# Kernel optimization log

Hardware: AMD Instinct MI355X
Metric: run time of the kernel (lower is better)

## Reference

```python
import jax, jax.numpy as jnp
import numpy as np

NUM_HEADS = 16
KEY_DIM = 64
EPS = 1e-6


def setup_inputs() -> dict:
    key = jax.random.key(0)
    k0, k1, k2, k3, k4 = jax.random.split(key, 5)
    B, S, E = 4, 4096, NUM_HEADS * KEY_DIM
    scale = 1.0 / np.sqrt(KEY_DIM)
    return {
        "query": jax.random.normal(k0, (B, S, E), dtype=jnp.float32),
        "Wq": jax.random.normal(k1, (NUM_HEADS, KEY_DIM, KEY_DIM), dtype=jnp.float32) * scale,
        "Wk": jax.random.normal(k2, (NUM_HEADS, KEY_DIM, KEY_DIM), dtype=jnp.float32) * scale,
        "Wv": jax.random.normal(k3, (NUM_HEADS, KEY_DIM, KEY_DIM), dtype=jnp.float32) * scale,
        "Wo": jax.random.normal(k4, (E, E), dtype=jnp.float32) * (1.0 / np.sqrt(E)),
    }


def reference(query, Wq, Wk, Wv, Wo):
    # Self-attention: key = value = query (per call() defaults).
    B, S, E = query.shape
    H, D = NUM_HEADS, KEY_DIM
    # split_heads: (B, S, E) -> (B, H, S, D)
    x = jnp.transpose(query.reshape(B, S, H, D), (0, 2, 1, 3))
    # Per-head linear projections (all heads batched in one einsum each).
    q = jnp.einsum("bhsd,hde->bhse", x, Wq)
    k = jnp.einsum("bhsd,hde->bhse", x, Wk)
    v = jnp.einsum("bhsd,hde->bhse", x, Wv)
    # Kernel feature map phi(x) = elu(x) + 1 (strictly positive).
    phi_q = jax.nn.elu(q) + 1.0
    phi_k = jax.nn.elu(k) + 1.0
    # Linear (non-causal) attention: O(S*D^2) instead of O(S^2*D).
    kv = jnp.einsum("bhsd,bhse->bhde", phi_k, v)        # (B,H,D,D)
    k_sum = jnp.sum(phi_k, axis=2)                       # (B,H,D)
    z = jnp.einsum("bhsd,bhd->bhs", phi_q, k_sum)        # (B,H,S)
    ctx = jnp.einsum("bhsd,bhde->bhse", phi_q, kv) / (z[..., None] + EPS)
    # combine_heads: (B,H,S,D) -> (B,S,E), then output projection (no bias).
    combined = jnp.transpose(ctx, (0, 2, 1, 3)).reshape(B, S, H * D)
    return combined @ Wo
```

## Files before the change

kernel.cpp:

```cpp
#include <hip/hip_runtime.h>
#include <stdint.h>

#define S_LEN 4096
#define NHEADS 16
#define DHEAD 64
#define EMB 1024
#define NBATCH 4
#define NBH (NBATCH * NHEADS)

typedef unsigned short u16t;
typedef __attribute__((ext_vector_type(8))) short short8;
typedef __attribute__((ext_vector_type(4))) float f32x4;

__device__ __forceinline__ u16t f2bf(float f) {
  unsigned int x = __float_as_uint(f);
  x += 0x7fffu + ((x >> 16) & 1u);
  return (u16t)(x >> 16);
}
__device__ __forceinline__ unsigned int pack2(float a, float b) {
  return (unsigned int)f2bf(a) | ((unsigned int)f2bf(b) << 16);
}
__device__ __forceinline__ float bf2f(u16t u) { return __uint_as_float(((unsigned int)u) << 16); }
__device__ __forceinline__ float phifn(float v) { return v > 0.f ? v + 1.f : __expf(v); }

__device__ __forceinline__ void stage_w8k(const u16t* __restrict__ wg,
                                          u16t* __restrict__ lds, int t) {
#pragma unroll
  for (int c = 0; c < 2; ++c) {
    const u16t* src = wg + (size_t)(c * 256 + t) * 8;
    char* dst = (char*)lds + c * 4096 + ((t >> 6) << 10);
    __builtin_amdgcn_global_load_lds((const __attribute__((address_space(1))) unsigned int*)src,
                                     (__attribute__((address_space(3))) unsigned int*)dst,
                                     16, 0, 0);
  }
}

__global__ __launch_bounds__(256) void la_prep(const float* __restrict__ Wq,
                                               const float* __restrict__ Wk,
                                               const float* __restrict__ Wv,
                                               u16t* __restrict__ WqT,
                                               u16t* __restrict__ WkT,
                                               u16t* __restrict__ WvT) {
  __shared__ float tmp[64][65];
  int blk = blockIdx.x;
  int mat = blk >> 4, h = blk & 15;
  const float* src = (mat == 0 ? Wq : (mat == 1 ? Wk : Wv)) + (size_t)h * 4096;
  u16t* dst = (mat == 0 ? WqT : (mat == 1 ? WkT : WvT)) + (size_t)h * 4096;
  int t = threadIdx.x;
#pragma unroll
  for (int p = 0; p < 16; ++p) {
    int i = p * 256 + t;
    tmp[i >> 6][i & 63] = src[i];
  }
  __syncthreads();
#pragma unroll
  for (int p = 0; p < 16; ++p) {
    int i = p * 256 + t;
    int e = i >> 6, r = i & 63, o = r >> 3, j = r & 7;
    dst[i] = f2bf(tmp[((o ^ (e & 7)) << 3) + j][e]);
  }
}

__global__ __launch_bounds__(256) void la_wot(const float* __restrict__ Wo,
                                              u16t* __restrict__ WoT) {
  __shared__ float t[64][65];
  int n0 = blockIdx.x * 64, k0 = blockIdx.y * 64;
  int tx = threadIdx.x, ty = threadIdx.y;
  for (int r = ty; r < 64; r += 4) t[r][tx] = Wo[(size_t)(k0 + r) * EMB + n0 + tx];
  __syncthreads();
  for (int r = ty; r < 64; r += 4)
    WoT[(size_t)(n0 + r) * EMB + k0 + tx] = f2bf(t[tx][r]);
}

__global__ __launch_bounds__(256) void la_kvq4(const float* __restrict__ q,
                                               const u16t* __restrict__ WqT,
                                               const u16t* __restrict__ WkT,
                                               const u16t* __restrict__ WvT,
                                               u16t* __restrict__ phiq,
                                               float* __restrict__ kvpart,
                                               float* __restrict__ kspart) {
  __shared__ u16t xs[128 * 72];
  __shared__ u16t wq[4096];
  __shared__ u16t wk[4096];
  __shared__ u16t wv[4096];
  __shared__ u16t pkT[64 * 136];
  __shared__ u16t vT[64 * 136];
  __shared__ float ksp4[4][64];
  int blk = blockIdx.x;
  int bh = blk >> 3, tile = blk & 7;
  int b = bh >> 4, h = bh & 15;
  int s0 = tile << 9;
  int t = threadIdx.x;
  int wave = t >> 6, lane = t & 63, l16 = lane & 15, g = lane >> 4;

  stage_w8k(WqT + (size_t)h * 4096, wq, t);
  stage_w8k(WkT + (size_t)h * 4096, wk, t);
  stage_w8k(WvT + (size_t)h * 4096, wv, t);

  const float* xg = q + ((size_t)b * S_LEN + s0) * EMB + h * 64;
  int pr_r = t >> 4, pr_c4 = (t & 15) * 4;

  float4 pre[8];
#pragma unroll
  for (int i = 0; i < 8; ++i)
    pre[i] = *(const float4*)(xg + (size_t)(i * 16 + pr_r) * EMB + pr_c4);

  f32x4 kacc[4];
#pragma unroll
  for (int n = 0; n < 4; ++n) kacc[n] = 0.f;
  float ks_acc = 0.f;
  int ks_e = t & 63, ks_q = t >> 6;

  for (int c = 0; c < 4; ++c) {
    if (c) __syncthreads();
#pragma unroll
    for (int i = 0; i < 8; ++i) {
      uint2 p;
      p.x = pack2(pre[i].x, pre[i].y);
      p.y = pack2(pre[i].z, pre[i].w);
      *(uint2*)(&xs[(i * 16 + pr_r) * 72 + pr_c4]) = p;
    }
    if (c < 3) {
#pragma unroll
      for (int i = 0; i < 8; ++i)
        pre[i] = *(const float4*)(xg + (size_t)((c + 1) * 128 + i * 16 + pr_r) * EMB + pr_c4);
    }
    __syncthreads();

    f32x4 aQ[2][4], aK[2][4], aV[2][4];
#pragma unroll
    for (int m = 0; m < 2; ++m)
#pragma unroll
      for (int n = 0; n < 4; ++n) { aQ[m][n] = 0.f; aK[m][n] = 0.f; aV[m][n] = 0.f; }
    short8 af[2][2];
#pragma unroll
    for (int m = 0; m < 2; ++m)
#pragma unroll
      for (int kk = 0; kk < 2; ++kk)
        af[m][kk] = *(const short8*)(&xs[(wave * 32 + m * 16 + l16) * 72 + kk * 32 + g * 8]);
#pragma unroll
    for (int n = 0; n < 4; ++n) {
      int e = n * 16 + l16;
#pragma unroll
      for (int kk = 0; kk < 2; ++kk) {
        int op = (kk * 4 + g) ^ (l16 & 7);
        short8 bQ = *(const short8*)(&wq[e * 64 + op * 8]);
        short8 bK = *(const short8*)(&wk[e * 64 + op * 8]);
        short8 bV = *(const short8*)(&wv[e * 64 + op * 8]);
#pragma unroll
        for (int m = 0; m < 2; ++m) {
          aQ[m][n] = __builtin_amdgcn_mfma_f32_16x16x32_bf16(af[m][kk], bQ, aQ[m][n], 0, 0, 0);
          aK[m][n] = __builtin_amdgcn_mfma_f32_16x16x32_bf16(af[m][kk], bK, aK[m][n], 0, 0, 0);
          aV[m][n] = __builtin_amdgcn_mfma_f32_16x16x32_bf16(af[m][kk], bV, aV[m][n], 0, 0, 0);
        }
      }
    }
    __syncthreads();

#pragma unroll
    for (int m = 0; m < 2; ++m)
#pragma unroll
      for (int n = 0; n < 4; ++n) {
        int e = n * 16 + l16;
        int sb = wave * 32 + m * 16 + g * 4;
        uint2 pk2, vv2;
        pk2.x = pack2(phifn(aK[m][n][0]), phifn(aK[m][n][1]));
        pk2.y = pack2(phifn(aK[m][n][2]), phifn(aK[m][n][3]));
        vv2.x = pack2(aV[m][n][0], aV[m][n][1]);
        vv2.y = pack2(aV[m][n][2], aV[m][n][3]);
        *(uint2*)(&pkT[e * 136 + sb]) = pk2;
        *(uint2*)(&vT[e * 136 + sb]) = vv2;
#pragma unroll
        for (int j = 0; j < 4; ++j) xs[(sb + j) * 72 + e] = f2bf(phifn(aQ[m][n][j]));
      }
    __syncthreads();

#pragma unroll
    for (int i = 0; i < 4; ++i) {
      int slot = i * 256 + t;
      int r = slot >> 3, cc = (slot & 7) * 8;
      *(uint4*)(phiq + ((size_t)bh * S_LEN + s0 + c * 128 + r) * 64 + cc) =
          *(const uint4*)(&xs[r * 72 + cc]);
    }
#pragma unroll
    for (int ks = 0; ks < 4; ++ks) {
      short8 pa = *(const short8*)(&pkT[(wave * 16 + l16) * 136 + ks * 32 + g * 8]);
#pragma unroll
      for (int n = 0; n < 4; ++n) {
        short8 vb = *(const short8*)(&vT[(n * 16 + l16) * 136 + ks * 32 + g * 8]);
        kacc[n] = __builtin_amdgcn_mfma_f32_16x16x32_bf16(pa, vb, kacc[n], 0, 0, 0);
      }
    }
#pragma unroll
    for (int i = 0; i < 8; ++i) {
      uint2 u = *(const uint2*)(&pkT[ks_e * 136 + ks_q * 32 + i * 4]);
      ks_acc += bf2f((u16t)(u.x & 0xffff)) + bf2f((u16t)(u.x >> 16)) +
                bf2f((u16t)(u.y & 0xffff)) + bf2f((u16t)(u.y >> 16));
    }
  }

  float* kp = kvpart + (size_t)blk * 4096;
#pragma unroll
  for (int n = 0; n < 4; ++n)
#pragma unroll
    for (int j = 0; j < 4; ++j)
      kp[(wave * 16 + g * 4 + j) * 64 + n * 16 + l16] = kacc[n][j];

  ksp4[ks_q][ks_e] = ks_acc;
  __syncthreads();
  if (t < 64)
    kspart[(size_t)blk * 64 + t] = ksp4[0][t] + ksp4[1][t] + ksp4[2][t] + ksp4[3][t];
}

__global__ __launch_bounds__(256) void la_red3(const float* __restrict__ kvpart,
                                               const float* __restrict__ kspart,
                                               const u16t* __restrict__ WoT,
                                               float* __restrict__ ksum_g,
                                               u16t* __restrict__ W2T) {
  __shared__ float kvs[64][65];
  __shared__ u16t aT[256 * 72];
  int bh = blockIdx.x;
  int b = bh >> 4, h = bh & 15;
  int t = threadIdx.x, wave = t >> 6, lane = t & 63, l16 = lane & 15, g = lane >> 4;

  float acc[16];
#pragma unroll
  for (int i = 0; i < 16; ++i) acc[i] = 0.f;
  for (int p = 0; p < 8; ++p) {
    const float* base = kvpart + ((size_t)bh * 8 + p) * 4096;
#pragma unroll
    for (int i = 0; i < 16; ++i) acc[i] += base[i * 256 + t];
  }
#pragma unroll
  for (int i = 0; i < 16; ++i) {
    int idx = i * 256 + t;
    kvs[idx >> 6][idx & 63] = acc[i];
  }
  if (t < 64) {
    float a = 0.f;
    for (int p = 0; p < 8; ++p) a += kspart[((size_t)bh * 8 + p) * 64 + t];
    ksum_g[(size_t)bh * 64 + t] = a;
  }
  __syncthreads();

  short8 kvbf[4][2];
#pragma unroll
  for (int n = 0; n < 4; ++n)
#pragma unroll
    for (int kk = 0; kk < 2; ++kk) {
      u16t* pp = (u16t*)&kvbf[n][kk];
#pragma unroll
      for (int i = 0; i < 8; ++i) pp[i] = f2bf(kvs[n * 16 + l16][kk * 32 + g * 8 + i]);
    }

  for (int ec = 0; ec < 4; ++ec) {
    if (ec) __syncthreads();
#pragma unroll
    for (int p = 0; p < 8; ++p) {
      int slot = p * 256 + t;
      int r = slot >> 3, cc = (slot & 7) * 8;
      *(uint4*)(&aT[r * 72 + cc]) =
          *(const uint4*)(WoT + (size_t)(ec * 256 + r) * 1024 + h * 64 + cc);
    }
    __syncthreads();
    f32x4 c2[4][4];
#pragma unroll
    for (int mi = 0; mi < 4; ++mi)
#pragma unroll
      for (int n = 0; n < 4; ++n) c2[mi][n] = 0.f;
#pragma unroll
    for (int kk = 0; kk < 2; ++kk)
#pragma unroll
      for (int mi = 0; mi < 4; ++mi) {
        short8 afr = *(const short8*)(&aT[(wave * 64 + mi * 16 + l16) * 72 + kk * 32 + g * 8]);
#pragma unroll
        for (int n = 0; n < 4; ++n)
          c2[mi][n] = __builtin_amdgcn_mfma_f32_16x16x32_bf16(afr, kvbf[n][kk], c2[mi][n], 0, 0, 0);
      }
    __syncthreads();
#pragma unroll
    for (int mi = 0; mi < 4; ++mi)
#pragma unroll
      for (int n = 0; n < 4; ++n)
#pragma unroll
        for (int j = 0; j < 4; ++j)
          aT[(wave * 64 + mi * 16 + g * 4 + j) * 72 + n * 16 + l16] = f2bf(c2[mi][n][j]);
    __syncthreads();
#pragma unroll
    for (int p = 0; p < 8; ++p) {
      int slot = p * 256 + t;
      int r = slot >> 3, cc = (slot & 7) * 8;
      *(uint4*)(W2T + ((size_t)b << 20) + (size_t)(ec * 256 + r) * 1024 + h * 64 + cc) =
          *(const uint4*)(&aT[r * 72 + cc]);
    }
  }
}

__global__ __launch_bounds__(256) void la_scale(const u16t* __restrict__ phiq,
                                                const float* __restrict__ ksum_g,
                                                u16t* __restrict__ phiq2) {
  __shared__ float ks[64];
  int blk = blockIdx.x;
  int bh = blk >> 4, sl = blk & 15;
  int b = bh >> 4, h = bh & 15;
  int s0 = sl * 256;
  int t = threadIdx.x;
  if (t < 64) ks[t] = ksum_g[(size_t)bh * 64 + t];
  __syncthreads();
  int c16 = t & 15, rg = t >> 4;
#pragma unroll 2
  for (int it = 0; it < 16; ++it) {
    int s = s0 + it * 16 + rg;
    uint2 u = *(const uint2*)(phiq + ((size_t)bh * S_LEN + s) * 64 + c16 * 4);
    float f0 = bf2f((u16t)(u.x & 0xffff)), f1 = bf2f((u16t)(u.x >> 16));
    float f2 = bf2f((u16t)(u.y & 0xffff)), f3 = bf2f((u16t)(u.y >> 16));
    float zp = f0 * ks[c16 * 4] + f1 * ks[c16 * 4 + 1] + f2 * ks[c16 * 4 + 2] + f3 * ks[c16 * 4 + 3];
    zp += __shfl_xor(zp, 1);
    zp += __shfl_xor(zp, 2);
    zp += __shfl_xor(zp, 4);
    zp += __shfl_xor(zp, 8);
    float inv = 1.f / (zp + 1e-6f);
    uint2 o;
    o.x = pack2(f0 * inv, f1 * inv);
    o.y = pack2(f2 * inv, f3 * inv);
    *(uint2*)(phiq2 + ((size_t)(b * S_LEN + s)) * EMB + h * 64 + c16 * 4) = o;
  }
}

__device__ __forceinline__ void stage_half(const u16t* __restrict__ gbase,
                                           u16t* __restrict__ lbuf,
                                           int half, int t) {
#pragma unroll
  for (int it = 0; it < 2; ++it) {
    int slot = it * 512 + t;
    int row = half * 128 + (slot >> 3);
    int oct = slot & 7;
    const u16t* src = gbase + (size_t)row * EMB + (((oct ^ (row & 7)) << 3));
    char* dst = (char*)lbuf + ((half * 128 + it * 64 + ((t >> 6) << 3)) << 7);
    __builtin_amdgcn_global_load_lds((const __attribute__((address_space(1))) unsigned int*)src,
                                     (__attribute__((address_space(3))) unsigned int*)dst,
                                     16, 0, 0);
  }
}

#define GFENCE asm volatile("" ::: "memory")

#define LOAD_A(QM)                                                              \
  _Pragma("unroll") for (int mi = 0; mi < 4; ++mi) _Pragma("unroll")            \
      for (int kk = 0; kk < 2; ++kk) {                                          \
    int rr = (QM) * 128 + wr2 * 64 + mi * 16 + l16;                             \
    afr[mi][kk] = *(const short8*)((const char*)Acur + rr * 128 +               \
                                   ((((kk << 2) | g) ^ (rr & 7)) << 4));        \
  }
#define LOAD_B(QN, DST)                                                         \
  _Pragma("unroll") for (int ni = 0; ni < 2; ++ni) _Pragma("unroll")            \
      for (int kk = 0; kk < 2; ++kk) {                                          \
    int rr = (QN) * 128 + wc2 * 32 + ni * 16 + l16;                             \
    DST[ni][kk] = *(const short8*)((const char*)Bcur + rr * 128 +               \
                                   ((((kk << 2) | g) ^ (rr & 7)) << 4));        \
  }
#define MFMA_Q(QM, QN, BF)                                                      \
  __builtin_amdgcn_s_setprio(1);                                                \
  _Pragma("unroll") for (int mi = 0; mi < 4; ++mi) _Pragma("unroll")            \
      for (int ni = 0; ni < 2; ++ni) {                                          \
    acc[QM][QN][mi][ni] = __builtin_amdgcn_mfma_f32_16x16x32_bf16(              \
        afr[mi][0], BF[ni][0], acc[QM][QN][mi][ni], 0, 0, 0);                   \
    acc[QM][QN][mi][ni] = __builtin_amdgcn_mfma_f32_16x16x32_bf16(              \
        afr[mi][1], BF[ni][1], acc[QM][QN][mi][ni], 0, 0, 0);                   \
  }                                                                             \
  __builtin_amdgcn_s_setprio(0);

#define BAR()                      \
  __builtin_amdgcn_s_barrier();    \
  GFENCE

__global__ __launch_bounds__(512, 2) void la_gemm9(const u16t* __restrict__ A,
                                                   const u16t* __restrict__ W2T,
                                                   float* __restrict__ C) {
  __shared__ u16t Al[2][16384];
  __shared__ u16t Bl[2][16384];
  int t = threadIdx.x;
  int bid = blockIdx.x;
  int swz = ((bid & 7) << 5) + (bid >> 3);
  int mt = swz >> 2, nt = swz & 3;
  const int M0 = mt * 256, N0 = nt * 256;
  const int b = mt >> 4;
  int wave = t >> 6, lane = t & 63;
  int l16 = lane & 15, g = lane >> 4;
  int wr2 = wave >> 2, wc2 = wave & 3;

  f32x4 acc[2][2][4][2];
#pragma unroll
  for (int qm = 0; qm < 2; ++qm)
#pragma unroll
    for (int qn = 0; qn < 2; ++qn)
#pragma unroll
      for (int mi = 0; mi < 4; ++mi)
#pragma unroll
        for (int ni = 0; ni < 2; ++ni) acc[qm][qn][mi][ni] = 0.f;

  const u16t* Asrc = A + (size_t)M0 * EMB;
  const u16t* Bsrc = W2T + ((size_t)b << 20) + (size_t)N0 * EMB;

  stage_half(Asrc, Al[0], 0, t);
  stage_half(Bsrc, Bl[0], 0, t);
  stage_half(Bsrc, Bl[0], 1, t);
  stage_half(Asrc, Al[0], 1, t);
  asm volatile("s_waitcnt vmcnt(4)" ::: "memory");
  BAR();

  short8 afr[4][2], bf0[2][2], bf1[2][2];

  for (int kt = 0; kt < 15; ++kt) {
    const u16t* Acur = Al[kt & 1];
    const u16t* Bcur = Bl[kt & 1];
    u16t* Anxt = Al[(kt + 1) & 1];
    u16t* Bnxt = Bl[(kt + 1) & 1];
    const u16t* An = Asrc + (kt + 1) * 64;
    const u16t* Bn = Bsrc + (kt + 1) * 64;
    LOAD_A(0);
    LOAD_B(0, bf0);
    stage_half(An, Anxt, 0, t);
    stage_half(Bn, Bnxt, 0, t);
    asm volatile("s_waitcnt vmcnt(6)" ::: "memory");
    BAR();
    MFMA_Q(0, 0, bf0);
    GFENCE;
    BAR();
    LOAD_B(1, bf1);
    stage_half(Bn, Bnxt, 1, t);
    asm volatile("s_waitcnt vmcnt(6)" ::: "memory");
    BAR();
    MFMA_Q(0, 1, bf1);
    GFENCE;
    BAR();
    LOAD_A(1);
    stage_half(An, Anxt, 1, t);
    BAR();
    MFMA_Q(1, 1, bf1);
    GFENCE;
    BAR();
    asm volatile("s_waitcnt vmcnt(4)" ::: "memory");
    BAR();
    MFMA_Q(1, 0, bf0);
    GFENCE;
    BAR();
  }
  {
    const u16t* Acur = Al[1];
    const u16t* Bcur = Bl[1];
    LOAD_A(0);
    LOAD_B(0, bf0);
    asm volatile("s_waitcnt vmcnt(2)" ::: "memory");
    BAR();
    MFMA_Q(0, 0, bf0);
    GFENCE;
    BAR();
    LOAD_B(1, bf1);
    asm volatile("s_waitcnt vmcnt(0)" ::: "memory");
    BAR();
    MFMA_Q(0, 1, bf1);
    GFENCE;
    BAR();
    LOAD_A(1);
    BAR();
    MFMA_Q(1, 1, bf1);
    GFENCE;
    BAR();
    BAR();
    MFMA_Q(1, 0, bf0);
    GFENCE;
  }

#pragma unroll
  for (int qm = 0; qm < 2; ++qm)
#pragma unroll
    for (int qn = 0; qn < 2; ++qn)
#pragma unroll
      for (int mi = 0; mi < 4; ++mi)
#pragma unroll
        for (int ni = 0; ni < 2; ++ni)
#pragma unroll
          for (int j = 0; j < 4; ++j) {
            int row = M0 + qm * 128 + wr2 * 64 + mi * 16 + g * 4 + j;
            int col = N0 + qn * 128 + wc2 * 32 + ni * 16 + l16;
            C[(size_t)row * EMB + col] = acc[qm][qn][mi][ni][j];
          }
}

extern "C" void kernel_launch(void* const* d_in, const int* in_sizes, int n_in,
                              void* d_out, int out_size, void* d_ws, size_t ws_size,
                              hipStream_t stream) {
  const float* query = (const float*)d_in[0];
  const float* Wq = (const float*)d_in[1];
  const float* Wk = (const float*)d_in[2];
  const float* Wv = (const float*)d_in[3];
  const float* Wo = (const float*)d_in[4];
  float* out = (float*)d_out;
  char* ws = (char*)d_ws;

  u16t* WoT     = (u16t*)(ws);
  u16t* WqT     = (u16t*)(ws + 2097152);
  u16t* WkT     = (u16t*)(ws + 2228224);
  u16t* WvT     = (u16t*)(ws + 2359296);
  u16t* phiq    = (u16t*)(ws + 2490368);
  float* kvpart = (float*)(ws + 36044800);
  float* kspart = (float*)(ws + 44433408);
  float* ksum_g = (float*)(ws + 44564480);
  u16t* W2T     = (u16t*)(ws + 44580864);
  u16t* phiq2   = (u16t*)(ws + 52969472);

  la_prep<<<48, 256, 0, stream>>>(Wq, Wk, Wv, WqT, WkT, WvT);
  la_wot<<<dim3(16, 16), dim3(64, 4), 0, stream>>>(Wo, WoT);
  la_kvq4<<<512, 256, 0, stream>>>(query, WqT, WkT, WvT, phiq, kvpart, kspart);
  la_red3<<<NBH, 256, 0, stream>>>(kvpart, kspart, WoT, ksum_g, W2T);
  la_scale<<<1024, 256, 0, stream>>>(phiq, ksum_g, phiq2);
  la_gemm9<<<256, 512, 0, stream>>>(phiq2, W2T, out);
}
```

Measured before the change: 112.1 us.

## Merge weight prep kernels, halve kvq chunk size, stage GEMM epilogue through LDS

Merges the Wq/Wk/Wv transpose kernel and the Wo transpose kernel into one launch, removing one kernel launch. The projection kernel now processes 64-row chunks instead of 128-row chunks, which cuts LDS and register use (possibly raising occupancy) at the cost of twice as many loop iterations and barriers. The final GEMM writes its accumulators through shared memory so the global stores become coalesced float4 rows instead of scattered scalar stores, adding extra barriers and LDS traffic.

```diff
diff --git a/kernel.cpp b/kernel.cpp
--- a/kernel.cpp
+++ b/kernel.cpp
@@ -35,56 +35,57 @@
   }
 }
 
-__global__ __launch_bounds__(256) void la_prep(const float* __restrict__ Wq,
-                                               const float* __restrict__ Wk,
-                                               const float* __restrict__ Wv,
-                                               u16t* __restrict__ WqT,
-                                               u16t* __restrict__ WkT,
-                                               u16t* __restrict__ WvT) {
+__global__ __launch_bounds__(256) void la_wprep(const float* __restrict__ Wq,
+                                                const float* __restrict__ Wk,
+                                                const float* __restrict__ Wv,
+                                                const float* __restrict__ Wo,
+                                                u16t* __restrict__ WqT,
+                                                u16t* __restrict__ WkT,
+                                                u16t* __restrict__ WvT,
+                                                u16t* __restrict__ WoT) {
   __shared__ float tmp[64][65];
   int blk = blockIdx.x;
-  int mat = blk >> 4, h = blk & 15;
-  const float* src = (mat == 0 ? Wq : (mat == 1 ? Wk : Wv)) + (size_t)h * 4096;
-  u16t* dst = (mat == 0 ? WqT : (mat == 1 ? WkT : WvT)) + (size_t)h * 4096;
   int t = threadIdx.x;
-#pragma unroll
-  for (int p = 0; p < 16; ++p) {
-    int i = p * 256 + t;
-    tmp[i >> 6][i & 63] = src[i];
-  }
-  __syncthreads();
-#pragma unroll
-  for (int p = 0; p < 16; ++p) {
-    int i = p * 256 + t;
-    int e = i >> 6, r = i & 63, o = r >> 3, j = r & 7;
-    dst[i] = f2bf(tmp[((o ^ (e & 7)) << 3) + j][e]);
-  }
-}
-
-__global__ __launch_bounds__(256) void la_wot(const float* __restrict__ Wo,
-                                              u16t* __restrict__ WoT) {
-  __shared__ float t[64][65];
-  int n0 = blockIdx.x * 64, k0 = blockIdx.y * 64;
-  int tx = threadIdx.x, ty = threadIdx.y;
-  for (int r = ty; r < 64; r += 4) t[r][tx] = Wo[(size_t)(k0 + r) * EMB + n0 + tx];
-  __syncthreads();
-  for (int r = ty; r < 64; r += 4)
-    WoT[(size_t)(n0 + r) * EMB + k0 + tx] = f2bf(t[tx][r]);
-}
-
-__global__ __launch_bounds__(256) void la_kvq4(const float* __restrict__ q,
+  if (blk < 48) {
+    int mat = blk >> 4, h = blk & 15;
+    const float* src = (mat == 0 ? Wq : (mat == 1 ? Wk : Wv)) + (size_t)h * 4096;
+    u16t* dst = (mat == 0 ? WqT : (mat == 1 ? WkT : WvT)) + (size_t)h * 4096;
+#pragma unroll
+    for (int p = 0; p < 16; ++p) {
+      int i = p * 256 + t;
+      tmp[i >> 6][i & 63] = src[i];
+    }
+    __syncthreads();
+#pragma unroll
+    for (int p = 0; p < 16; ++p) {
+      int i = p * 256 + t;
+      int e = i >> 6, r = i & 63, o = r >> 3, j = r & 7;
+      dst[i] = f2bf(tmp[((o ^ (e & 7)) << 3) + j][e]);
+    }
+  } else {
+    int bb = blk - 48;
+    int n0 = (bb & 15) * 64, k0 = (bb >> 4) * 64;
+    int tx = t & 63, ty = t >> 6;
+    for (int r = ty; r < 64; r += 4) tmp[r][tx] = Wo[(size_t)(k0 + r) * EMB + n0 + tx];
+    __syncthreads();
+    for (int r = ty; r < 64; r += 4)
+      WoT[(size_t)(n0 + r) * EMB + k0 + tx] = f2bf(tmp[tx][r]);
+  }
+}
+
+__global__ __launch_bounds__(256) void la_kvq5(const float* __restrict__ q,
                                                const u16t* __restrict__ WqT,
                                                const u16t* __restrict__ WkT,
                                                const u16t* __restrict__ WvT,
                                                u16t* __restrict__ phiq,
                                                float* __restrict__ kvpart,
                                                float* __restrict__ kspart) {
-  __shared__ u16t xs[128 * 72];
+  __shared__ u16t xs[64 * 72];
   __shared__ u16t wq[4096];
   __shared__ u16t wk[4096];
   __shared__ u16t wv[4096];
-  __shared__ u16t pkT[64 * 136];
-  __shared__ u16t vT[64 * 136];
+  __shared__ u16t pkT[64 * 72];
+  __shared__ u16t vT[64 * 72];
   __shared__ float ksp4[4][64];
   int blk = blockIdx.x;
   int bh = blk >> 3, tile = blk & 7;
@@ -100,9 +101,9 @@
   const float* xg = q + ((size_t)b * S_LEN + s0) * EMB + h * 64;
   int pr_r = t >> 4, pr_c4 = (t & 15) * 4;
 
-  float4 pre[8];
-#pragma unroll
-  for (int i = 0; i < 8; ++i)
+  float4 pre[4];
+#pragma unroll
+  for (int i = 0; i < 4; ++i)
     pre[i] = *(const float4*)(xg + (size_t)(i * 16 + pr_r) * EMB + pr_c4);
 
   f32x4 kacc[4];
@@ -111,33 +112,29 @@
   float ks_acc = 0.f;
   int ks_e = t & 63, ks_q = t >> 6;
 
-  for (int c = 0; c < 4; ++c) {
+  for (int c = 0; c < 8; ++c) {
     if (c) __syncthreads();
 #pragma unroll
-    for (int i = 0; i < 8; ++i) {
+    for (int i = 0; i < 4; ++i) {
       uint2 p;
       p.x = pack2(pre[i].x, pre[i].y);
       p.y = pack2(pre[i].z, pre[i].w);
       *(uint2*)(&xs[(i * 16 + pr_r) * 72 + pr_c4]) = p;
     }
-    if (c < 3) {
-#pragma unroll
-      for (int i = 0; i < 8; ++i)
-        pre[i] = *(const float4*)(xg + (size_t)((c + 1) * 128 + i * 16 + pr_r) * EMB + pr_c4);
-    }
-    __syncthreads();
-
-    f32x4 aQ[2][4], aK[2][4], aV[2][4];
-#pragma unroll
-    for (int m = 0; m < 2; ++m)
-#pragma unroll
-      for (int n = 0; n < 4; ++n) { aQ[m][n] = 0.f; aK[m][n] = 0.f; aV[m][n] = 0.f; }
-    short8 af[2][2];
-#pragma unroll
-    for (int m = 0; m < 2; ++m)
-#pragma unroll
-      for (int kk = 0; kk < 2; ++kk)
-        af[m][kk] = *(const short8*)(&xs[(wave * 32 + m * 16 + l16) * 72 + kk * 32 + g * 8]);
+    if (c < 7) {
+#pragma unroll
+      for (int i = 0; i < 4; ++i)
+        pre[i] = *(const float4*)(xg + (size_t)((c + 1) * 64 + i * 16 + pr_r) * EMB + pr_c4);
+    }
+    __syncthreads();
+
+    f32x4 aQ[4], aK[4], aV[4];
+#pragma unroll
+    for (int n = 0; n < 4; ++n) { aQ[n] = 0.f; aK[n] = 0.f; aV[n] = 0.f; }
+    short8 af[2];
+#pragma unroll
+    for (int kk = 0; kk < 2; ++kk)
+      af[kk] = *(const short8*)(&xs[(wave * 16 + l16) * 72 + kk * 32 + g * 8]);
 #pragma unroll
     for (int n = 0; n < 4; ++n) {
       int e = n * 16 + l16;
@@ -147,53 +144,48 @@
         short8 bQ = *(const short8*)(&wq[e * 64 + op * 8]);
         short8 bK = *(const short8*)(&wk[e * 64 + op * 8]);
         short8 bV = *(const short8*)(&wv[e * 64 + op * 8]);
-#pragma unroll
-        for (int m = 0; m < 2; ++m) {
-          aQ[m][n] = __builtin_amdgcn_mfma_f32_16x16x32_bf16(af[m][kk], bQ, aQ[m][n], 0, 0, 0);
-          aK[m][n] = __builtin_amdgcn_mfma_f32_16x16x32_bf16(af[m][kk], bK, aK[m][n], 0, 0, 0);
-          aV[m][n] = __builtin_amdgcn_mfma_f32_16x16x32_bf16(af[m][kk], bV, aV[m][n], 0, 0, 0);
-        }
+        aQ[n] = __builtin_amdgcn_mfma_f32_16x16x32_bf16(af[kk], bQ, aQ[n], 0, 0, 0);
+        aK[n] = __builtin_amdgcn_mfma_f32_16x16x32_bf16(af[kk], bK, aK[n], 0, 0, 0);
+        aV[n] = __builtin_amdgcn_mfma_f32_16x16x32_bf16(af[kk], bV, aV[n], 0, 0, 0);
       }
     }
     __syncthreads();
 
 #pragma unroll
-    for (int m = 0; m < 2; ++m)
-#pragma unroll
-      for (int n = 0; n < 4; ++n) {
-        int e = n * 16 + l16;
-        int sb = wave * 32 + m * 16 + g * 4;
-        uint2 pk2, vv2;
-        pk2.x = pack2(phifn(aK[m][n][0]), phifn(aK[m][n][1]));
-        pk2.y = pack2(phifn(aK[m][n][2]), phifn(aK[m][n][3]));
-        vv2.x = pack2(aV[m][n][0], aV[m][n][1]);
-        vv2.y = pack2(aV[m][n][2], aV[m][n][3]);
-        *(uint2*)(&pkT[e * 136 + sb]) = pk2;
-        *(uint2*)(&vT[e * 136 + sb]) = vv2;
-#pragma unroll
-        for (int j = 0; j < 4; ++j) xs[(sb + j) * 72 + e] = f2bf(phifn(aQ[m][n][j]));
-      }
-    __syncthreads();
-
-#pragma unroll
-    for (int i = 0; i < 4; ++i) {
+    for (int n = 0; n < 4; ++n) {
+      int e = n * 16 + l16;
+      int sb = wave * 16 + g * 4;
+      uint2 pk2, vv2;
+      pk2.x = pack2(phifn(aK[n][0]), phifn(aK[n][1]));
+      pk2.y = pack2(phifn(aK[n][2]), phifn(aK[n][3]));
+      vv2.x = pack2(aV[n][0], aV[n][1]);
+      vv2.y = pack2(aV[n][2], aV[n][3]);
+      *(uint2*)(&pkT[e * 72 + sb]) = pk2;
+      *(uint2*)(&vT[e * 72 + sb]) = vv2;
+#pragma unroll
+      for (int j = 0; j < 4; ++j) xs[(sb + j) * 72 + e] = f2bf(phifn(aQ[n][j]));
+    }
+    __syncthreads();
+
+#pragma unroll
+    for (int i = 0; i < 2; ++i) {
       int slot = i * 256 + t;
       int r = slot >> 3, cc = (slot & 7) * 8;
-      *(uint4*)(phiq + ((size_t)bh * S_LEN + s0 + c * 128 + r) * 64 + cc) =
+      *(uint4*)(phiq + ((size_t)bh * S_LEN + s0 + c * 64 + r) * 64 + cc) =
           *(const uint4*)(&xs[r * 72 + cc]);
     }
 #pragma unroll
-    for (int ks = 0; ks < 4; ++ks) {
-      short8 pa = *(const short8*)(&pkT[(wave * 16 + l16) * 136 + ks * 32 + g * 8]);
+    for (int ks = 0; ks < 2; ++ks) {
+      short8 pa = *(const short8*)(&pkT[(wave * 16 + l16) * 72 + ks * 32 + g * 8]);
 #pragma unroll
       for (int n = 0; n < 4; ++n) {
-        short8 vb = *(const short8*)(&vT[(n * 16 + l16) * 136 + ks * 32 + g * 8]);
+        short8 vb = *(const short8*)(&vT[(n * 16 + l16) * 72 + ks * 32 + g * 8]);
         kacc[n] = __builtin_amdgcn_mfma_f32_16x16x32_bf16(pa, vb, kacc[n], 0, 0, 0);
       }
     }
 #pragma unroll
-    for (int i = 0; i < 8; ++i) {
-      uint2 u = *(const uint2*)(&pkT[ks_e * 136 + ks_q * 32 + i * 4]);
+    for (int i = 0; i < 4; ++i) {
+      uint2 u = *(const uint2*)(&pkT[ks_e * 72 + ks_q * 16 + i * 4]);
       ks_acc += bf2f((u16t)(u.x & 0xffff)) + bf2f((u16t)(u.x >> 16)) +
                 bf2f((u16t)(u.y & 0xffff)) + bf2f((u16t)(u.y >> 16));
     }
@@ -377,8 +369,11 @@
 __global__ __launch_bounds__(512, 2) void la_gemm9(const u16t* __restrict__ A,
                                                    const u16t* __restrict__ W2T,
                                                    float* __restrict__ C) {
-  __shared__ u16t Al[2][16384];
-  __shared__ u16t Bl[2][16384];
+  __shared__ u16t SMEM[65536];
+  u16t* Al0 = SMEM;
+  u16t* Al1 = SMEM + 16384;
+  u16t* Bl0 = SMEM + 32768;
+  u16t* Bl1 = SMEM + 49152;
   int t = threadIdx.x;
   int bid = blockIdx.x;
   int swz = ((bid & 7) << 5) + (bid >> 3);
@@ -402,20 +397,20 @@
   const u16t* Asrc = A + (size_t)M0 * EMB;
   const u16t* Bsrc = W2T + ((size_t)b << 20) + (size_t)N0 * EMB;
 
-  stage_half(Asrc, Al[0], 0, t);
-  stage_half(Bsrc, Bl[0], 0, t);
-  stage_half(Bsrc, Bl[0], 1, t);
-  stage_half(Asrc, Al[0], 1, t);
+  stage_half(Asrc, Al0, 0, t);
+  stage_half(Bsrc, Bl0, 0, t);
+  stage_half(Bsrc, Bl0, 1, t);
+  stage_half(Asrc, Al0, 1, t);
   asm volatile("s_waitcnt vmcnt(4)" ::: "memory");
   BAR();
 
   short8 afr[4][2], bf0[2][2], bf1[2][2];
 
   for (int kt = 0; kt < 15; ++kt) {
-    const u16t* Acur = Al[kt & 1];
-    const u16t* Bcur = Bl[kt & 1];
-    u16t* Anxt = Al[(kt + 1) & 1];
-    u16t* Bnxt = Bl[(kt + 1) & 1];
+    const u16t* Acur = (kt & 1) ? Al1 : Al0;
+    const u16t* Bcur = (kt & 1) ? Bl1 : Bl0;
+    u16t* Anxt = (kt & 1) ? Al0 : Al1;
+    u16t* Bnxt = (kt & 1) ? Bl0 : Bl1;
     const u16t* An = Asrc + (kt + 1) * 64;
     const u16t* Bn = Bsrc + (kt + 1) * 64;
     LOAD_A(0);
@@ -447,8 +442,8 @@
     BAR();
   }
   {
-    const u16t* Acur = Al[1];
-    const u16t* Bcur = Bl[1];
+    const u16t* Acur = Al1;
+    const u16t* Bcur = Bl1;
     LOAD_A(0);
     LOAD_B(0, bf0);
     asm volatile("s_waitcnt vmcnt(2)" ::: "memory");
@@ -472,20 +467,31 @@
     GFENCE;
   }
 
-#pragma unroll
-  for (int qm = 0; qm < 2; ++qm)
-#pragma unroll
-    for (int qn = 0; qn < 2; ++qn)
-#pragma unroll
-      for (int mi = 0; mi < 4; ++mi)
-#pragma unroll
-        for (int ni = 0; ni < 2; ++ni)
-#pragma unroll
-          for (int j = 0; j < 4; ++j) {
-            int row = M0 + qm * 128 + wr2 * 64 + mi * 16 + g * 4 + j;
-            int col = N0 + qn * 128 + wc2 * 32 + ni * 16 + l16;
-            C[(size_t)row * EMB + col] = acc[qm][qn][mi][ni][j];
-          }
+  float* cs = (float*)SMEM;
+  BAR();
+#pragma unroll
+  for (int qq = 0; qq < 4; ++qq) {
+    int qm = qq >> 1, qn = qq & 1;
+#pragma unroll
+    for (int mi = 0; mi < 4; ++mi)
+#pragma unroll
+      for (int ni = 0; ni < 2; ++ni)
+#pragma unroll
+        for (int j = 0; j < 4; ++j) {
+          int row = wr2 * 64 + mi * 16 + g * 4 + j;
+          int col = wc2 * 32 + ni * 16 + l16;
+          cs[row * 132 + col] = acc[qm][qn][mi][ni][j];
+        }
+    BAR();
+#pragma unroll
+    for (int i = 0; i < 8; ++i) {
+      int slot = i * 512 + t;
+      int r = slot >> 5, sg = slot & 31;
+      float4 v = *(const float4*)(&cs[r * 132 + sg * 4]);
+      *(float4*)(&C[(size_t)(M0 + qm * 128 + r) * EMB + N0 + qn * 128 + sg * 4]) = v;
+    }
+    BAR();
+  }
 }
 
 extern "C" void kernel_launch(void* const* d_in, const int* in_sizes, int n_in,
@@ -510,9 +516,8 @@
   u16t* W2T     = (u16t*)(ws + 44580864);
   u16t* phiq2   = (u16t*)(ws + 52969472);
 
-  la_prep<<<48, 256, 0, stream>>>(Wq, Wk, Wv, WqT, WkT, WvT);
-  la_wot<<<dim3(16, 16), dim3(64, 4), 0, stream>>>(Wo, WoT);
-  la_kvq4<<<512, 256, 0, stream>>>(query, WqT, WkT, WvT, phiq, kvpart, kspart);
+  la_wprep<<<304, 256, 0, stream>>>(Wq, Wk, Wv, Wo, WqT, WkT, WvT, WoT);
+  la_kvq5<<<512, 256, 0, stream>>>(query, WqT, WkT, WvT, phiq, kvpart, kspart);
   la_red3<<<NBH, 256, 0, stream>>>(kvpart, kspart, WoT, ksum_g, W2T);
   la_scale<<<1024, 256, 0, stream>>>(phiq, ksum_g, phiq2);
   la_gemm9<<<256, 512, 0, stream>>>(phiq2, W2T, out);
```

Measured after the change: 106.7 us. -4.8%, faster.
